# Kernel tuning notes

Hardware: AMD Instinct MI355X
Metric: run time of the kernel (lower is better)

Reference implementation:

```python
import jax, jax.numpy as jnp
import numpy as np

B, T = 64, 8192
VOCAB = 50257
MAX_PHRASE_LEN = 32
PAD_ID = 0


def setup_inputs() -> dict:
    key = jax.random.key(0)
    k1, k2, k3, k4 = jax.random.split(key, 4)
    input_ids = jax.random.randint(k1, (B, T), 1, VOCAB, dtype=jnp.int32)
    # realistic right-padding: each row has a random real length in [T/2, T]
    lengths = jax.random.randint(k4, (B,), T // 2, T + 1, dtype=jnp.int32)
    pos = jnp.arange(T, dtype=jnp.int32)
    input_ids = jnp.where(pos[None, :] < lengths[:, None], input_ids, PAD_ID)
    is_punct = jax.random.uniform(k2, (VOCAB,)) < 0.06
    is_punct = is_punct.at[PAD_ID].set(False)
    is_abbreviation = jax.random.uniform(k3, (VOCAB,)) < 0.01
    return {"input_ids": input_ids, "is_punct": is_punct, "is_abbreviation": is_abbreviation}


def reference(input_ids, is_punct, is_abbreviation):
    Bs, Ts = input_ids.shape
    max_phrase_len = MAX_PHRASE_LEN
    pad_token_id = PAD_ID

    # ---- compute_is_end ----
    punct_at_t = is_punct[input_ids]                                   # [B,T]
    prev_ids = jnp.concatenate(
        [jnp.zeros((Bs, 1), input_ids.dtype), input_ids[:, :-1]], axis=1)
    prev_is_abbr = is_abbreviation[prev_ids].at[:, 0].set(False)
    is_real = input_ids != pad_token_id
    base_end = punct_at_t & ~prev_is_abbr & is_real                    # [B,T]

    pos = jnp.arange(Ts, dtype=jnp.int32)
    last_real = jnp.max(jnp.where(is_real, pos[None, :], -1), axis=1)  # [B]

    def step(last_boundary, xs):
        t, e = xs  # t scalar, e [B]
        at_last = last_real == t
        forced = (t - last_boundary) >= max_phrase_len
        fire = (e | at_last | forced) & (t <= last_real)
        new_lb = jnp.where(fire, t, last_boundary)
        return new_lb, fire

    init_lb = jnp.full((Bs,), -1, dtype=jnp.int32)
    _, fires = jax.lax.scan(step, init_lb, (pos, base_end.T))
    is_end = fires.T                                                   # [B,T]

    # ---- pack_phrases_from_is_end ----
    # static upper bound on phrase count (torch uses phrase_id.max()+1)
    P = Ts
    ie = is_end.astype(jnp.int32)
    phrase_id = jnp.concatenate(
        [jnp.zeros((Bs, 1), jnp.int32), jnp.cumsum(ie[:, :-1], axis=1)], axis=1)  # [B,T]
    pos2 = jnp.broadcast_to(pos[None, :], (Bs, Ts))
    brow = jnp.arange(Bs, dtype=jnp.int32)[:, None]

    # segment-min of position per phrase (scatter_reduce amin)
    first_pos = jnp.full((Bs, P), Ts, dtype=jnp.int32).at[brow, phrase_id].min(pos2)
    slot = pos2 - jnp.take_along_axis(first_pos, phrase_id, axis=1)    # [B,T]
    in_range = (slot < max_phrase_len) & (slot >= 0) & is_real

    # invalid entries get an out-of-bounds slot -> dropped by scatter
    slot_safe = jnp.where(in_range, slot, max_phrase_len)
    bidx = jnp.broadcast_to(brow, (Bs, Ts))
    phrase_mask = jnp.zeros((Bs, P, max_phrase_len), dtype=bool).at[
        bidx, phrase_id, slot_safe].set(True, mode='drop')
    phrase_token_idx = jnp.zeros((Bs, P, max_phrase_len), dtype=jnp.int32).at[
        bidx, phrase_id, slot_safe].set(pos2, mode='drop')

    end_src = jnp.where(in_range, pos2, -1)
    phrase_end_pos = jnp.full((Bs, P), -1, dtype=jnp.int32).at[brow, phrase_id].max(end_src)

    return phrase_mask, phrase_token_idx, phrase_end_pos, phrase_id
```

## Files before the change

### kernel.cpp

```cpp
#include <hip/hip_runtime.h>
#include <stdint.h>

typedef unsigned long long ull;

#define Bdim 64
#define Tdim 8192
#define MAXP 32
#define NW (Tdim / 64)
#define VOCAB_WORDS_MAX 1024

__global__ void detect_layout_kernel(const int* __restrict__ p, int nwords,
                                     unsigned long long* __restrict__ flag) {
    __shared__ int s_max;
    if (threadIdx.x == 0) s_max = 0;
    __syncthreads();
    int m = 0;
    for (int i = threadIdx.x; i < nwords; i += blockDim.x) {
        int v = p[i];
        if (v < 0) v = 2;
        if (v > m) m = v;
    }
    atomicMax(&s_max, m);
    __syncthreads();
    if (threadIdx.x == 0) *flag = (s_max > 1) ? 1ull : 0ull;
}

__global__ void pack_bits_kernel(const void* __restrict__ punct,
                                 const void* __restrict__ abbr,
                                 int vocab,
                                 const unsigned long long* __restrict__ flag,
                                 unsigned long long* __restrict__ pbits,
                                 unsigned long long* __restrict__ abits,
                                 int nwords) {
    int w = blockIdx.x * blockDim.x + threadIdx.x;
    if (w >= nwords) return;
    bool u8 = (*flag != 0ull);
    unsigned long long pw = 0ull, aw = 0ull;
    int base = w << 6;
    for (int j = 0; j < 64; ++j) {
        int tok = base + j;
        if (tok >= vocab) break;
        bool pv, av;
        if (u8) {
            pv = ((const uint8_t*)punct)[tok] != 0;
            av = ((const uint8_t*)abbr)[tok] != 0;
        } else {
            pv = ((const int*)punct)[tok] != 0;
            av = ((const int*)abbr)[tok] != 0;
        }
        if (pv) pw |= 1ull << j;
        if (av) aw |= 1ull << j;
    }
    pbits[w] = pw;
    abits[w] = aw;
}

__global__ __launch_bounds__(1024) void phrase_meta_kernel(
    const int* __restrict__ ids,
    const unsigned long long* __restrict__ pbits,
    const unsigned long long* __restrict__ abits,
    int* __restrict__ out_end,
    int* __restrict__ out_pid,
    unsigned int* __restrict__ ws_nb,
    unsigned int* __restrict__ ws_info)
{
    __shared__ ull base_bits[NW];
    __shared__ ull end_bits[NW];
    __shared__ int A_pref[NW];
    __shared__ int wpre[NW];
    __shared__ int E_pref[NW];
    __shared__ int s_last;

    const int b = blockIdx.x;
    const int tid = threadIdx.x;
    const int lane = tid & 63;
    const int wv = tid >> 6;
    const int* __restrict__ row = ids + (size_t)b * Tdim;
    const size_t rowbase = (size_t)b * Tdim;

    if (tid == 0) s_last = -1;
    __syncthreads();

    int lmax = -1;
#pragma unroll
    for (int k = 0; k < Tdim / 1024; ++k) {
        int t = k * 1024 + tid;
        int id = row[t];
        bool real = (id != 0);
        bool pu = (pbits[id >> 6] >> (id & 63)) & 1ull;
        bool ab = false;
        if (t > 0) {
            int pv = row[t - 1];
            ab = (abits[pv >> 6] >> (pv & 63)) & 1ull;
        }
        bool be = pu && !ab && real;
        ull bal = __ballot(be);
        if (lane == 0) base_bits[k * 16 + wv] = bal;
        if (real) lmax = t;
        out_end[rowbase + t] = -1;
    }
    for (int off = 32; off; off >>= 1) {
        int o = __shfl_down(lmax, off);
        lmax = o > lmax ? o : lmax;
    }
    if (lane == 0) atomicMax(&s_last, lmax);
    __syncthreads();

    if (tid == 0) {
        int run = -1;
#pragma unroll 8
        for (int w = 0; w < NW; ++w) {
            A_pref[w] = run;
            ull x = base_bits[w];
            if (x) run = (w << 6) + 63 - __builtin_clzll(x);
        }
    }
    __syncthreads();

    const int LR = s_last;
#pragma unroll
    for (int k = 0; k < Tdim / 1024; ++k) {
        int t = k * 1024 + tid;
        int w = k * 16 + wv;
        ull bw = base_bits[w];
        ull below = bw & ((1ull << lane) - 1ull);
        int pa = below ? ((w << 6) + 63 - __builtin_clzll(below)) : A_pref[w];
        bool bnd = (t <= LR) &&
                   (((bw >> lane) & 1ull) || (t == LR) || (((t - pa) & 31) == 0));
        ull bal = __ballot(bnd);
        if (lane == 0) end_bits[w] = bal;
    }
    __syncthreads();

    if (tid == 0) {
        int run = -1, cnt = 0;
#pragma unroll 8
        for (int w = 0; w < NW; ++w) {
            wpre[w] = cnt;
            E_pref[w] = run;
            ull x = end_bits[w];
            cnt += __builtin_popcountll(x);
            if (x) run = (w << 6) + 63 - __builtin_clzll(x);
        }
        ws_nb[b] = (unsigned int)cnt;
    }
    __syncthreads();

#pragma unroll
    for (int k = 0; k < Tdim / 1024; ++k) {
        int t = k * 1024 + tid;
        int w = k * 16 + wv;
        ull ew = end_bits[w];
        ull below = ew & ((1ull << lane) - 1ull);
        int pid = wpre[w] + __builtin_popcountll(below);
        out_pid[rowbase + t] = pid;
        if ((ew >> lane) & 1ull) {
            int pe = below ? ((w << 6) + 63 - __builtin_clzll(below)) : E_pref[w];
            int first = pe + 1;
            ws_info[(size_t)b * Tdim + pid] =
                (unsigned int)first | ((unsigned int)t << 16);
            out_end[rowbase + pid] = t;
        }
    }
}

__global__ __launch_bounds__(256) void fill_outputs_kernel(
    const unsigned int* __restrict__ ws_nb,
    const unsigned int* __restrict__ ws_info,
    int4* __restrict__ m4,
    int4* __restrict__ i4)
{
    const int row = blockIdx.x >> 5;
    const int seg = blockIdx.x & 31;
    const int nb = (int)ws_nb[row];
    const unsigned int* __restrict__ info = ws_info + (size_t)row * Tdim;
    int4* __restrict__ mrow = m4 + (size_t)row * 65536;
    int4* __restrict__ irow = i4 + (size_t)row * 65536;
#pragma unroll
    for (int i = 0; i < 8; ++i) {
        int g = seg * 2048 + i * 256 + (int)threadIdx.x;
        int pid = g >> 3;
        int s0 = (g & 7) << 2;
        int4 mv = {0, 0, 0, 0};
        int4 iv = {0, 0, 0, 0};
        if (pid < nb) {
            unsigned int u = info[pid];
            int first = (int)(u & 0xFFFFu);
            int len = (int)(u >> 16) - first + 1;
            mv.x = (s0 + 0) < len;
            mv.y = (s0 + 1) < len;
            mv.z = (s0 + 2) < len;
            mv.w = (s0 + 3) < len;
            iv.x = (s0 + 0) < len ? first + s0 + 0 : 0;
            iv.y = (s0 + 1) < len ? first + s0 + 1 : 0;
            iv.z = (s0 + 2) < len ? first + s0 + 2 : 0;
            iv.w = (s0 + 3) < len ? first + s0 + 3 : 0;
        }
        mrow[g] = mv;
        irow[g] = iv;
    }
}

extern "C" void kernel_launch(void* const* d_in, const int* in_sizes, int n_in,
                              void* d_out, int out_size, void* d_ws, size_t ws_size,
                              hipStream_t stream) {
    const int* ids = (const int*)d_in[0];
    const void* punct = d_in[1];
    const void* abbr = d_in[2];
    const int vocab = in_sizes[1];

    int* out = (int*)d_out;
    const size_t maskN = (size_t)Bdim * Tdim * MAXP;
    int* out_mask = out;
    int* out_idx  = out + maskN;
    int* out_end  = out + 2 * maskN;
    int* out_pid  = out + 2 * maskN + (size_t)Bdim * Tdim;

    unsigned long long* flag  = (unsigned long long*)d_ws;
    unsigned long long* pbits = (unsigned long long*)((char*)d_ws + 64);
    unsigned long long* abits = pbits + VOCAB_WORDS_MAX;
    unsigned int* ws_nb   = (unsigned int*)(abits + VOCAB_WORDS_MAX);
    unsigned int* ws_info = ws_nb + 64;

    detect_layout_kernel<<<1, 256, 0, stream>>>((const int*)punct, vocab / 4, flag);

    const int nwords = (vocab + 63) / 64;
    pack_bits_kernel<<<(nwords + 255) / 256, 256, 0, stream>>>(
        punct, abbr, vocab, flag, pbits, abits, nwords);

    phrase_meta_kernel<<<Bdim, 1024, 0, stream>>>(
        ids, pbits, abits, out_end, out_pid, ws_nb, ws_info);

    fill_outputs_kernel<<<Bdim * 32, 256, 0, stream>>>(
        ws_nb, ws_info, (int4*)out_mask, (int4*)out_idx);
}
```

Measured before the change: 206.2 us.

## Merge table-packing kernels and parallelize per-row prefix scans with wave shuffles

The layout-detection and bit-packing kernels are merged into one single-block kernel, which removes one launch and the global flag round-trip. The serial single-thread loops over 128 words that build A_pref, wpre and E_pref are replaced by a 64-lane shuffle-based inclusive scan, with two words per lane. This shortens the serial critical path inside phrase_meta_kernel. In exchange, the packing now runs in one block of 1024 threads, where before it used several blocks.

```diff
diff --git a/kernel.cpp b/kernel.cpp
--- a/kernel.cpp
+++ b/kernel.cpp
@@ -9,56 +9,54 @@
 #define NW (Tdim / 64)
 #define VOCAB_WORDS_MAX 1024
 
-__global__ void detect_layout_kernel(const int* __restrict__ p, int nwords,
-                                     unsigned long long* __restrict__ flag) {
-    __shared__ int s_max;
-    if (threadIdx.x == 0) s_max = 0;
-    __syncthreads();
+__global__ __launch_bounds__(1024) void pack_tables_kernel(
+    const void* __restrict__ punct,
+    const void* __restrict__ abbr,
+    int vocab,
+    ull* __restrict__ pbits,
+    ull* __restrict__ abits) {
+    __shared__ int s_flag;
+    if (threadIdx.x == 0) s_flag = 0;
+    __syncthreads();
+
+    const unsigned* p32 = (const unsigned*)punct;
+    const int nw32 = vocab >> 2;
     int m = 0;
-    for (int i = threadIdx.x; i < nwords; i += blockDim.x) {
-        int v = p[i];
-        if (v < 0) v = 2;
-        if (v > m) m = v;
-    }
-    atomicMax(&s_max, m);
-    __syncthreads();
-    if (threadIdx.x == 0) *flag = (s_max > 1) ? 1ull : 0ull;
-}
-
-__global__ void pack_bits_kernel(const void* __restrict__ punct,
-                                 const void* __restrict__ abbr,
-                                 int vocab,
-                                 const unsigned long long* __restrict__ flag,
-                                 unsigned long long* __restrict__ pbits,
-                                 unsigned long long* __restrict__ abits,
-                                 int nwords) {
-    int w = blockIdx.x * blockDim.x + threadIdx.x;
-    if (w >= nwords) return;
-    bool u8 = (*flag != 0ull);
-    unsigned long long pw = 0ull, aw = 0ull;
-    int base = w << 6;
-    for (int j = 0; j < 64; ++j) {
-        int tok = base + j;
-        if (tok >= vocab) break;
-        bool pv, av;
-        if (u8) {
-            pv = ((const uint8_t*)punct)[tok] != 0;
-            av = ((const uint8_t*)abbr)[tok] != 0;
-        } else {
-            pv = ((const int*)punct)[tok] != 0;
-            av = ((const int*)abbr)[tok] != 0;
-        }
-        if (pv) pw |= 1ull << j;
-        if (av) aw |= 1ull << j;
-    }
-    pbits[w] = pw;
-    abits[w] = aw;
+    for (int i = threadIdx.x; i < nw32; i += 1024) {
+        if (p32[i] > 1u) m = 1;
+    }
+    if (m) atomicOr(&s_flag, 1);
+    __syncthreads();
+    const bool u8 = (s_flag != 0);
+
+    const int nwords = (vocab + 63) >> 6;
+    for (int w = threadIdx.x; w < nwords; w += 1024) {
+        ull pw = 0ull, aw = 0ull;
+        const int base = w << 6;
+#pragma unroll 1
+        for (int j = 0; j < 64; ++j) {
+            int tok = base + j;
+            if (tok >= vocab) break;
+            bool pv, av;
+            if (u8) {
+                pv = ((const uint8_t*)punct)[tok] != 0;
+                av = ((const uint8_t*)abbr)[tok] != 0;
+            } else {
+                pv = ((const int*)punct)[tok] != 0;
+                av = ((const int*)abbr)[tok] != 0;
+            }
+            if (pv) pw |= 1ull << j;
+            if (av) aw |= 1ull << j;
+        }
+        pbits[w] = pw;
+        abits[w] = aw;
+    }
 }
 
 __global__ __launch_bounds__(1024) void phrase_meta_kernel(
     const int* __restrict__ ids,
-    const unsigned long long* __restrict__ pbits,
-    const unsigned long long* __restrict__ abits,
+    const ull* __restrict__ pbits,
+    const ull* __restrict__ abits,
     int* __restrict__ out_end,
     int* __restrict__ out_pid,
     unsigned int* __restrict__ ws_nb,
@@ -106,14 +104,21 @@
     if (lane == 0) atomicMax(&s_last, lmax);
     __syncthreads();
 
-    if (tid == 0) {
-        int run = -1;
-#pragma unroll 8
-        for (int w = 0; w < NW; ++w) {
-            A_pref[w] = run;
-            ull x = base_bits[w];
-            if (x) run = (w << 6) + 63 - __builtin_clzll(x);
-        }
+    if (tid < 64) {
+        int w0 = tid * 2, w1 = w0 + 1;
+        ull x0 = base_bits[w0], x1 = base_bits[w1];
+        int h0 = x0 ? (w0 << 6) + 63 - __builtin_clzll(x0) : -1;
+        int h1 = x1 ? (w1 << 6) + 63 - __builtin_clzll(x1) : -1;
+        int inc = h1 > h0 ? h1 : h0;
+#pragma unroll
+        for (int off = 1; off < 64; off <<= 1) {
+            int o = __shfl_up(inc, off);
+            if (tid >= off && o > inc) inc = o;
+        }
+        int exc = __shfl_up(inc, 1);
+        if (tid == 0) exc = -1;
+        A_pref[w0] = exc;
+        A_pref[w1] = h0 > exc ? h0 : exc;
     }
     __syncthreads();
 
@@ -132,17 +137,32 @@
     }
     __syncthreads();
 
-    if (tid == 0) {
-        int run = -1, cnt = 0;
-#pragma unroll 8
-        for (int w = 0; w < NW; ++w) {
-            wpre[w] = cnt;
-            E_pref[w] = run;
-            ull x = end_bits[w];
-            cnt += __builtin_popcountll(x);
-            if (x) run = (w << 6) + 63 - __builtin_clzll(x);
-        }
-        ws_nb[b] = (unsigned int)cnt;
+    if (tid < 64) {
+        int w0 = tid * 2, w1 = w0 + 1;
+        ull x0 = end_bits[w0], x1 = end_bits[w1];
+        int c0 = __builtin_popcountll(x0);
+        int csum = c0 + __builtin_popcountll(x1);
+        int h0 = x0 ? (w0 << 6) + 63 - __builtin_clzll(x0) : -1;
+        int h1 = x1 ? (w1 << 6) + 63 - __builtin_clzll(x1) : -1;
+        int incC = csum;
+        int incH = h1 > h0 ? h1 : h0;
+#pragma unroll
+        for (int off = 1; off < 64; off <<= 1) {
+            int oC = __shfl_up(incC, off);
+            int oH = __shfl_up(incH, off);
+            if (tid >= off) {
+                incC += oC;
+                if (oH > incH) incH = oH;
+            }
+        }
+        int excC = __shfl_up(incC, 1);
+        int excH = __shfl_up(incH, 1);
+        if (tid == 0) { excC = 0; excH = -1; }
+        wpre[w0] = excC;
+        wpre[w1] = excC + c0;
+        E_pref[w0] = excH;
+        E_pref[w1] = h0 > excH ? h0 : excH;
+        if (tid == 63) ws_nb[b] = (unsigned int)incC;
     }
     __syncthreads();
 
@@ -216,17 +236,12 @@
     int* out_end  = out + 2 * maskN;
     int* out_pid  = out + 2 * maskN + (size_t)Bdim * Tdim;
 
-    unsigned long long* flag  = (unsigned long long*)d_ws;
-    unsigned long long* pbits = (unsigned long long*)((char*)d_ws + 64);
-    unsigned long long* abits = pbits + VOCAB_WORDS_MAX;
+    ull* pbits = (ull*)d_ws;
+    ull* abits = pbits + VOCAB_WORDS_MAX;
     unsigned int* ws_nb   = (unsigned int*)(abits + VOCAB_WORDS_MAX);
     unsigned int* ws_info = ws_nb + 64;
 
-    detect_layout_kernel<<<1, 256, 0, stream>>>((const int*)punct, vocab / 4, flag);
-
-    const int nwords = (vocab + 63) / 64;
-    pack_bits_kernel<<<(nwords + 255) / 256, 256, 0, stream>>>(
-        punct, abbr, vocab, flag, pbits, abits, nwords);
+    pack_tables_kernel<<<1, 1024, 0, stream>>>(punct, abbr, vocab, pbits, abits);
 
     phrase_meta_kernel<<<Bdim, 1024, 0, stream>>>(
         ids, pbits, abits, out_end, out_pid, ws_nb, ws_info);
```

Result: no change. 206.6 us (+0.2%).
